# Performance work log

Measured on AMD Instinct MI355X. Metric: run time of the kernel, lower is better.

The kernel has to match this reference:

```python
import jax, jax.numpy as jnp
import numpy as np

ACH_SCALE = 1.0  # default _ach_scale


def setup_inputs() -> dict:
    key = jax.random.key(0)
    ks = jax.random.split(key, 6)
    B, K, D, H = 16, 256, 128, 64
    particles = jax.random.normal(ks[0], (B, K, D), dtype=jnp.float32)
    positions = jax.random.normal(ks[1], (B, K, 2), dtype=jnp.float32)
    # nn.Linear(2D, H): weight [H, 2D], bias [H]; store transposed [2D, H]
    lim1 = 1.0 / np.sqrt(2 * D)
    W1 = jax.random.uniform(ks[2], (2 * D, H), minval=-lim1, maxval=lim1, dtype=jnp.float32)
    b1 = jax.random.uniform(ks[3], (H,), minval=-lim1, maxval=lim1, dtype=jnp.float32)
    lim2 = 1.0 / np.sqrt(H)
    W2 = jax.random.uniform(ks[4], (H, 1), minval=-lim2, maxval=lim2, dtype=jnp.float32)
    b2 = jax.random.uniform(ks[5], (1,), minval=-lim2, maxval=lim2, dtype=jnp.float32)
    return {"particles": particles, "positions": positions,
            "W1": W1, "b1": b1, "W2": W2, "b2": b2}


def reference(particles, positions, W1, b1, W2, b2):
    B, K, D = particles.shape
    # Split the first Linear: cat([pi, pj]) @ W1 == pi @ W1[:D] + pj @ W1[D:]
    hi = jnp.einsum('bkd,dh->bkh', particles, W1[:D])      # [B,K,H]
    hj = jnp.einsum('bkd,dh->bkh', particles, W1[D:])      # [B,K,H]
    h = hi[:, :, None, :] + hj[:, None, :, :] + b1          # [B,K,K,H]
    h = jax.nn.gelu(h, approximate=False)                   # torch GELU default = exact
    signed_dist = (jnp.einsum('bijh,ho->bijo', h, W2) + b2)[..., 0]  # [B,K,K]
    # true pairwise distances (safe sqrt to mirror torch norm at 0)
    diff = positions[:, :, None, :] - positions[:, None, :, :]       # [B,K,K,2]
    d2 = jnp.sum(diff * diff, axis=-1)
    true_dist = jnp.where(d2 > 0, jnp.sqrt(jnp.where(d2 > 0, d2, 1.0)), 0.0)
    contact_loss = jnp.mean((signed_dist - true_dist) ** 2) * ACH_SCALE
    return (signed_dist, contact_loss)
```

## Files before the change

### kernel.cpp

```cpp
#include <hip/hip_runtime.h>
#include <hip/hip_bf16.h>
#include <math.h>


#define Bn 16
#define Kn 256
#define Dn 128
#define Hn 64
#define NBLK 1024

__device__ __forceinline__ void gelu_acc(float x, float w, float& acc) {
    float u  = fmaf(x, -20598733.0f, 1064987473.0f);
    int   iu = (int)u;
    float e  = __builtin_bit_cast(float, iu);
    float d  = e + 1.0f;
    int   ir = 0x7EF311C3 - __builtin_bit_cast(int, d);
    float r0 = __builtin_bit_cast(float, ir);
    float r  = r0 * fmaf(-d, r0, 2.0f);
    acc = fmaf(x * r, w, acc);
}

__global__ __launch_bounds__(256) void kA(const float* __restrict__ particles,
                                          const float* __restrict__ W1,
                                          const float* __restrict__ b1,
                                          float* __restrict__ hi,
                                          float* __restrict__ hj) {
    __shared__ __align__(16) float w1a[Dn * Hn];
    __shared__ __align__(16) float w1b[Dn * Hn];
    __shared__ __align__(16) float ps[16][Dn];
    __shared__ __align__(16) float b1s[Hn];

    const int tid = threadIdx.x;
    const int row0 = blockIdx.x * 16;

    for (int idx = tid; idx < (Dn * Hn) / 4; idx += 256) {
        ((float4*)w1a)[idx] = ((const float4*)W1)[idx];
        ((float4*)w1b)[idx] = ((const float4*)(W1 + Dn * Hn))[idx];
    }
    for (int idx = tid; idx < (16 * Dn) / 4; idx += 256)
        ((float4*)&ps[0][0])[idx] = ((const float4*)(particles + row0 * Dn))[idx];
    if (tid < Hn / 4)
        ((float4*)b1s)[tid] = ((const float4*)b1)[tid];
    __syncthreads();

    const int r  = tid >> 4;
    const int h0 = (tid & 15) * 4;

    float4 ai = {0.f, 0.f, 0.f, 0.f};
    float4 aj = {0.f, 0.f, 0.f, 0.f};
#pragma unroll 8
    for (int d = 0; d < Dn; ++d) {
        const float p  = ps[r][d];
        const float4 wa = *(const float4*)&w1a[d * Hn + h0];
        const float4 wb = *(const float4*)&w1b[d * Hn + h0];
        ai.x = fmaf(p, wa.x, ai.x); ai.y = fmaf(p, wa.y, ai.y);
        ai.z = fmaf(p, wa.z, ai.z); ai.w = fmaf(p, wa.w, ai.w);
        aj.x = fmaf(p, wb.x, aj.x); aj.y = fmaf(p, wb.y, aj.y);
        aj.z = fmaf(p, wb.z, aj.z); aj.w = fmaf(p, wb.w, aj.w);
    }
    const float4 bb = *(const float4*)&b1s[h0];
    ai.x += bb.x; ai.y += bb.y; ai.z += bb.z; ai.w += bb.w;

    *(float4*)&hi[(row0 + r) * Hn + h0] = ai;
    *(float4*)&hj[(row0 + r) * Hn + h0] = aj;
}

__global__ __launch_bounds__(256) void kB(const float* __restrict__ hi,
                                          const float* __restrict__ hj,
                                          const float* __restrict__ positions,
                                          const float* __restrict__ W2,
                                          const float* __restrict__ b2,
                                          float* __restrict__ out,
                                          float* __restrict__ partials) {
    __shared__ __align__(16) float shi[32][68];
    __shared__ __align__(16) float shj[32][68];
    __shared__ __align__(16) float w2s[Hn];
    __shared__ float pix[32], piy[32], pjx[32], pjy[32];
    __shared__ float wsum[4];

    const int jt = blockIdx.x, it = blockIdx.y, b = blockIdx.z;
    const int tid = threadIdx.x;
    const int bi = b * Kn + it * 32;
    const int bj = b * Kn + jt * 32;

    for (int idx = tid; idx < 512; idx += 256) {
        const int rr = idx >> 4, c4 = (idx & 15) * 4;
        *(float4*)&shi[rr][c4] = *(const float4*)&hi[(bi + rr) * Hn + c4];
        *(float4*)&shj[rr][c4] = *(const float4*)&hj[(bj + rr) * Hn + c4];
    }
    if (tid < Hn / 4)
        ((float4*)w2s)[tid] = ((const float4*)W2)[tid];
    if (tid < 32) {
        pix[tid] = positions[(bi + tid) * 2 + 0];
        piy[tid] = positions[(bi + tid) * 2 + 1];
        pjx[tid] = positions[(bj + tid) * 2 + 0];
        pjy[tid] = positions[(bj + tid) * 2 + 1];
    }
    const float bb = b2[0];
    __syncthreads();

    const int ti = tid >> 4, tj = tid & 15;

    float acc00 = 0.f, acc01 = 0.f, acc10 = 0.f, acc11 = 0.f;
#pragma unroll
    for (int h = 0; h < Hn; h += 4) {
        const float4 a0 = *(const float4*)&shi[ti][h];
        const float4 a1 = *(const float4*)&shi[ti + 16][h];
        const float4 c0 = *(const float4*)&shj[tj][h];
        const float4 c1 = *(const float4*)&shj[tj + 16][h];
        const float4 w  = *(const float4*)&w2s[h];
        gelu_acc(a0.x + c0.x, w.x, acc00); gelu_acc(a0.y + c0.y, w.y, acc00);
        gelu_acc(a0.z + c0.z, w.z, acc00); gelu_acc(a0.w + c0.w, w.w, acc00);
        gelu_acc(a0.x + c1.x, w.x, acc01); gelu_acc(a0.y + c1.y, w.y, acc01);
        gelu_acc(a0.z + c1.z, w.z, acc01); gelu_acc(a0.w + c1.w, w.w, acc01);
        gelu_acc(a1.x + c0.x, w.x, acc10); gelu_acc(a1.y + c0.y, w.y, acc10);
        gelu_acc(a1.z + c0.z, w.z, acc10); gelu_acc(a1.w + c0.w, w.w, acc10);
        gelu_acc(a1.x + c1.x, w.x, acc11); gelu_acc(a1.y + c1.y, w.y, acc11);
        gelu_acc(a1.z + c1.z, w.z, acc11); gelu_acc(a1.w + c1.w, w.w, acc11);
    }
    const float sd00 = acc00 + bb, sd01 = acc01 + bb;
    const float sd10 = acc10 + bb, sd11 = acc11 + bb;

    const float xi0 = pix[ti], yi0 = piy[ti], xi1 = pix[ti + 16], yi1 = piy[ti + 16];
    const float xj0 = pjx[tj], yj0 = pjy[tj], xj1 = pjx[tj + 16], yj1 = pjy[tj + 16];
    const float d200 = (xi0-xj0)*(xi0-xj0) + (yi0-yj0)*(yi0-yj0);
    const float d201 = (xi0-xj1)*(xi0-xj1) + (yi0-yj1)*(yi0-yj1);
    const float d210 = (xi1-xj0)*(xi1-xj0) + (yi1-yj0)*(yi1-yj0);
    const float d211 = (xi1-xj1)*(xi1-xj1) + (yi1-yj1)*(yi1-yj1);
    const float td00 = (d200 > 0.f) ? sqrtf(d200) : 0.f;
    const float td01 = (d201 > 0.f) ? sqrtf(d201) : 0.f;
    const float td10 = (d210 > 0.f) ? sqrtf(d210) : 0.f;
    const float td11 = (d211 > 0.f) ? sqrtf(d211) : 0.f;

    const int i0 = it * 32 + ti, i1 = i0 + 16;
    const int j0 = jt * 32 + tj, j1 = j0 + 16;
    out[((b * Kn) + i0) * Kn + j0] = sd00;
    out[((b * Kn) + i0) * Kn + j1] = sd01;
    out[((b * Kn) + i1) * Kn + j0] = sd10;
    out[((b * Kn) + i1) * Kn + j1] = sd11;

    float v = (sd00 - td00) * (sd00 - td00) + (sd01 - td01) * (sd01 - td01)
            + (sd10 - td10) * (sd10 - td10) + (sd11 - td11) * (sd11 - td11);
#pragma unroll
    for (int off = 32; off > 0; off >>= 1) v += __shfl_down(v, off);
    if ((tid & 63) == 0) wsum[tid >> 6] = v;
    __syncthreads();
    if (tid == 0) {
        const int bid = (b * gridDim.y + it) * gridDim.x + jt;
        partials[bid] = (wsum[0] + wsum[1]) + (wsum[2] + wsum[3]);
    }
}

__global__ __launch_bounds__(256) void kC(const float* __restrict__ partials,
                                          float* __restrict__ loss_out) {
    __shared__ float s[256];
    const int tid = threadIdx.x;
    const float4* p4 = (const float4*)partials;
    const float4 x = p4[tid];
    s[tid] = (x.x + x.y) + (x.z + x.w);
    __syncthreads();
    for (int off = 128; off > 0; off >>= 1) {
        if (tid < off) s[tid] += s[tid + off];
        __syncthreads();
    }
    if (tid == 0)
        loss_out[0] = s[0] * (1.0f / (float)(Bn * Kn * Kn));
}

extern "C" void kernel_launch(void* const* d_in, const int* in_sizes, int n_in,
                              void* d_out, int out_size, void* d_ws, size_t ws_size,
                              hipStream_t stream) {
    const float* particles = (const float*)d_in[0];
    const float* positions = (const float*)d_in[1];
    const float* W1        = (const float*)d_in[2];
    const float* b1        = (const float*)d_in[3];
    const float* W2        = (const float*)d_in[4];
    const float* b2        = (const float*)d_in[5];

    float* out = (float*)d_out;
    float* ws  = (float*)d_ws;
    float* hi       = ws;
    float* hj       = ws + Bn * Kn * Hn;
    float* partials = ws + 2 * Bn * Kn * Hn;

    kA<<<dim3((Bn * Kn) / 16), dim3(256), 0, stream>>>(particles, W1, b1, hi, hj);
    kB<<<dim3(Kn / 32, Kn / 32, Bn), dim3(256), 0, stream>>>(hi, hj, positions, W2, b2,
                                                             out, partials);
    kC<<<dim3(1), dim3(256), 0, stream>>>(partials, out + (size_t)Bn * Kn * Kn);
}
```

Measured before the change: 27.84 us.

## Drop LDS staging of W1 in projection kernel, read weights directly from global

Result: no change. 28.32 us (+1.7%).

```diff
diff --git a/kernel.cpp b/kernel.cpp
--- a/kernel.cpp
+++ b/kernel.cpp
@@ -20,49 +20,36 @@
     acc = fmaf(x * r, w, acc);
 }
 
-__global__ __launch_bounds__(256) void kA(const float* __restrict__ particles,
+__global__ __launch_bounds__(512) void kA(const float* __restrict__ particles,
                                           const float* __restrict__ W1,
                                           const float* __restrict__ b1,
                                           float* __restrict__ hi,
                                           float* __restrict__ hj) {
-    __shared__ __align__(16) float w1a[Dn * Hn];
-    __shared__ __align__(16) float w1b[Dn * Hn];
-    __shared__ __align__(16) float ps[16][Dn];
-    __shared__ __align__(16) float b1s[Hn];
+    const int tid = threadIdx.x;
+    const int hg  = tid & 63;
+    const int rg  = __builtin_amdgcn_readfirstlane(tid >> 6);
+    const int row = blockIdx.x * 16 + rg * 2;
 
-    const int tid = threadIdx.x;
-    const int row0 = blockIdx.x * 16;
+    const float* __restrict__ p0 = particles + (size_t)row * Dn;
+    const float* __restrict__ p1 = p0 + Dn;
+    const float* __restrict__ wa = W1 + hg;
+    const float* __restrict__ wb = W1 + Dn * Hn + hg;
 
-    for (int idx = tid; idx < (Dn * Hn) / 4; idx += 256) {
-        ((float4*)w1a)[idx] = ((const float4*)W1)[idx];
-        ((float4*)w1b)[idx] = ((const float4*)(W1 + Dn * Hn))[idx];
-    }
-    for (int idx = tid; idx < (16 * Dn) / 4; idx += 256)
-        ((float4*)&ps[0][0])[idx] = ((const float4*)(particles + row0 * Dn))[idx];
-    if (tid < Hn / 4)
-        ((float4*)b1s)[tid] = ((const float4*)b1)[tid];
-    __syncthreads();
-
-    const int r  = tid >> 4;
-    const int h0 = (tid & 15) * 4;
-
-    float4 ai = {0.f, 0.f, 0.f, 0.f};
-    float4 aj = {0.f, 0.f, 0.f, 0.f};
+    float ai0 = 0.f, ai1 = 0.f, aj0 = 0.f, aj1 = 0.f;
 #pragma unroll 8
     for (int d = 0; d < Dn; ++d) {
-        const float p  = ps[r][d];
-        const float4 wa = *(const float4*)&w1a[d * Hn + h0];
-        const float4 wb = *(const float4*)&w1b[d * Hn + h0];
-        ai.x = fmaf(p, wa.x, ai.x); ai.y = fmaf(p, wa.y, ai.y);
-        ai.z = fmaf(p, wa.z, ai.z); ai.w = fmaf(p, wa.w, ai.w);
-        aj.x = fmaf(p, wb.x, aj.x); aj.y = fmaf(p, wb.y, aj.y);
-        aj.z = fmaf(p, wb.z, aj.z); aj.w = fmaf(p, wb.w, aj.w);
+        const float pa = p0[d];
+        const float pb = p1[d];
+        const float va = wa[(size_t)d * Hn];
+        const float vb = wb[(size_t)d * Hn];
+        ai0 = fmaf(pa, va, ai0); ai1 = fmaf(pb, va, ai1);
+        aj0 = fmaf(pa, vb, aj0); aj1 = fmaf(pb, vb, aj1);
     }
-    const float4 bb = *(const float4*)&b1s[h0];
-    ai.x += bb.x; ai.y += bb.y; ai.z += bb.z; ai.w += bb.w;
-
-    *(float4*)&hi[(row0 + r) * Hn + h0] = ai;
-    *(float4*)&hj[(row0 + r) * Hn + h0] = aj;
+    const float bh = b1[hg];
+    hi[(size_t)row * Hn + hg]       = ai0 + bh;
+    hi[(size_t)(row + 1) * Hn + hg] = ai1 + bh;
+    hj[(size_t)row * Hn + hg]       = aj0;
+    hj[(size_t)(row + 1) * Hn + hg] = aj1;
 }
 
 __global__ __launch_bounds__(256) void kB(const float* __restrict__ hi,
@@ -183,7 +170,7 @@
     float* hj       = ws + Bn * Kn * Hn;
     float* partials = ws + 2 * Bn * Kn * Hn;
 
-    kA<<<dim3((Bn * Kn) / 16), dim3(256), 0, stream>>>(particles, W1, b1, hi, hj);
+    kA<<<dim3((Bn * Kn) / 16), dim3(512), 0, stream>>>(particles, W1, b1, hi, hj);
     kB<<<dim3(Kn / 32, Kn / 32, Bn), dim3(256), 0, stream>>>(hi, hj, positions, W2, b2,
                                                              out, partials);
     kC<<<dim3(1), dim3(256), 0, stream>>>(partials, out + (size_t)Bn * Kn * Kn);
```
